# Kernel tuning notes

Hardware: AMD Instinct MI355X
Metric: run time of the kernel (lower is better)

## Reference

```python
import jax, jax.numpy as jnp
import numpy as np

N_STATES = 2048   # number of hidden states
N_OBS = 8192      # emission alphabet size
T = 8192          # sequence length


def setup_inputs() -> dict:
    key = jax.random.key(0)
    k1, k2, k3, k4 = jax.random.split(key, 4)
    Pi_0 = jax.random.uniform(k1, (N_STATES,), jnp.float32)
    Pi_0 = Pi_0 / Pi_0.sum()  # initial distribution
    A = jax.random.uniform(k2, (N_STATES, N_STATES), jnp.float32)
    A = A / A.sum(axis=1, keepdims=True)  # row-stochastic transition matrix
    # emission values scaled so the per-step multiplicative factor has mean ~1,
    # keeping alpha numerically stable over T steps (the raw algorithm never rescales)
    B = jax.random.uniform(k3, (N_STATES, N_OBS), jnp.float32) * 2.0
    se = jax.random.randint(k4, (T,), 0, N_OBS)
    return {"Pi_0": Pi_0, "A": A, "B": B, "se": se}


def reference(Pi_0, A, B, se):
    # HMM forward algorithm:
    #   alpha_0[i] = Pi_0[i] * B[i, se[0]]
    #   alpha_t[i] = (sum_j alpha_{t-1}[j] * A[j, i]) * B[i, se[t]]
    #   return -log(sum_i alpha_T[i])
    Bobs = B[:, se].T            # [T, n_states] emission prob of each observed symbol
    alpha0 = Pi_0 * Bobs[0]      # [n_states]

    def step(alpha, b_t):
        alpha = (alpha @ A) * b_t  # vectorized recurrence: matvec + elementwise
        return alpha, None

    alpha, _ = jax.lax.scan(step, alpha0, Bobs[1:])
    return -jnp.log(jnp.sum(alpha))
```

## Files before the change

### kernel.cpp

```cpp
#include <hip/hip_runtime.h>
#include <math.h>


#define NS    2048
#define NOBS  8192
#define TSEQ  8192
#define NBLK  64
#define NTHR  512
#define OPB   32
#define JPT   128

typedef unsigned long long u64;
typedef unsigned int u32;

#define A_LIST(X) \
  X(0)  X(1)  X(2)  X(3)  X(4)  X(5)  X(6)  X(7)  \
  X(8)  X(9)  X(10) X(11) X(12) X(13) X(14) X(15) \
  X(16) X(17) X(18) X(19) X(20) X(21) X(22) X(23) \
  X(24) X(25) X(26) X(27) X(28) X(29) X(30) X(31)

__global__ void __launch_bounds__(256) init_ws_kernel(u64* aP) {
  const int i = threadIdx.x;
#pragma unroll
  for (int c = 0; c < 16; ++c) {
    __hip_atomic_store(&aP[i * 16 + c], 0ull, __ATOMIC_RELAXED, __HIP_MEMORY_SCOPE_AGENT);
  }
}

__global__ void __launch_bounds__(NTHR, 2) hmm_forward_kernel(
    const float* __restrict__ Pi0,
    const float* __restrict__ A,
    const float* __restrict__ B,
    const int*   __restrict__ se,
    float* __restrict__ out,
    u64*   __restrict__ aP) {
  __shared__ __align__(16) float alpha_sm[NS];
  __shared__ float red[2][NTHR / 64][OPB];

  const int tid    = threadIdx.x;
  const int blk    = blockIdx.x;
  const int w      = tid >> 6;
  const int lane   = tid & 63;
  const int h      = lane >> 5;
  const int o      = lane & 31;
  const int i_mine = blk * OPB + o;
  const int jbase  = (w * 2 + h) * JPT;

#define DECLA(k) float4 Ar##k;
  A_LIST(DECLA)
#define LOADA(k) { const float* ap = A + (size_t)(jbase + 4 * k) * NS + i_mine; \
                   Ar##k.x = ap[0]; Ar##k.y = ap[NS]; Ar##k.z = ap[2 * NS]; Ar##k.w = ap[3 * NS]; }
  A_LIST(LOADA)
#define PIN4(k) asm volatile("" : "+v"(Ar##k.x), "+v"(Ar##k.y), "+v"(Ar##k.z), "+v"(Ar##k.w));
  A_LIST(PIN4)

  {
    const int s0 = se[0];
#pragma unroll
    for (int c = 0; c < 4; ++c) {
      const int i = tid * 4 + c;
      alpha_sm[i] = Pi0[i] * B[(size_t)i * NOBS + s0];
    }
  }
  __syncthreads();

  float bv_next = 0.f;
  if (tid < OPB) bv_next = B[(size_t)i_mine * NOBS + se[1]];
  int sidx_n2 = se[2 < TSEQ ? 2 : TSEQ - 1];

  for (int t = 1; t < TSEQ; ++t) {
    const float bv  = bv_next;
    const int   buf = t & 1;
    if (tid < OPB) bv_next = B[(size_t)i_mine * NOBS + sidx_n2];
    {
      const int tn2 = (t + 2 < TSEQ) ? (t + 2) : (TSEQ - 1);
      sidx_n2 = se[tn2];
    }

    float a0 = 0.f, a1 = 0.f, a2 = 0.f, a3 = 0.f;
#define DOT(k) { const float4 av = *reinterpret_cast<const float4*>(&alpha_sm[jbase + 4 * k]); \
                 a0 = fmaf(Ar##k.x, av.x, a0); a1 = fmaf(Ar##k.y, av.y, a1); \
                 a2 = fmaf(Ar##k.z, av.z, a2); a3 = fmaf(Ar##k.w, av.w, a3); }
    A_LIST(DOT)
    float acc = (a0 + a1) + (a2 + a3);
    acc += __shfl_xor(acc, 32);
    if (lane < 32) red[buf][w][o] = acc;
    __syncthreads();

    if (w == 0) {
      __builtin_amdgcn_s_setprio(1);
      float s = 0.f;
#pragma unroll
      for (int ww = 0; ww < NTHR / 64; ++ww) s += red[buf][ww][o];
      if (lane < 32) {
        const float aval = s * bv;
        const u64 pkt = (u64)__float_as_uint(aval) | ((u64)(u32)t << 32);
        __hip_atomic_store(&aP[(size_t)buf * NS + blk * OPB + o], pkt,
                           __ATOMIC_RELAXED, __HIP_MEMORY_SCOPE_AGENT);
      }
      __builtin_amdgcn_s_setprio(0);
    }

    {
      const u64* src = aP + (size_t)buf * NS + w * 256 + lane * 4;
      u64 q0, q1, q2, q3;
      const u32 tag = (u32)t;
      for (;;) {
        q0 = __hip_atomic_load(&src[0], __ATOMIC_RELAXED, __HIP_MEMORY_SCOPE_AGENT);
        q1 = __hip_atomic_load(&src[1], __ATOMIC_RELAXED, __HIP_MEMORY_SCOPE_AGENT);
        q2 = __hip_atomic_load(&src[2], __ATOMIC_RELAXED, __HIP_MEMORY_SCOPE_AGENT);
        q3 = __hip_atomic_load(&src[3], __ATOMIC_RELAXED, __HIP_MEMORY_SCOPE_AGENT);
        if ((u32)(q0 >> 32) == tag && (u32)(q1 >> 32) == tag &&
            (u32)(q2 >> 32) == tag && (u32)(q3 >> 32) == tag) break;
      }
      float4 v;
      v.x = __uint_as_float((u32)q0);
      v.y = __uint_as_float((u32)q1);
      v.z = __uint_as_float((u32)q2);
      v.w = __uint_as_float((u32)q3);
      *reinterpret_cast<float4*>(&alpha_sm[w * 256 + lane * 4]) = v;
    }
  }

  if (blk == 0) {
    __syncthreads();
    float s = 0.f;
#pragma unroll
    for (int c = 0; c < 4; ++c) s += alpha_sm[4 * tid + c];
#pragma unroll
    for (int off = 32; off > 0; off >>= 1) s += __shfl_xor(s, off);
    if (lane == 0) red[0][w][0] = s;
    __syncthreads();
    if (tid == 0) {
      float S = 0.f;
#pragma unroll
      for (int ww = 0; ww < NTHR / 64; ++ww) S += red[0][ww][0];
      out[0] = -logf(S);
    }
  }
}

extern "C" void kernel_launch(void* const* d_in, const int* in_sizes, int n_in,
                              void* d_out, int out_size, void* d_ws, size_t ws_size,
                              hipStream_t stream) {
  const float* Pi0 = (const float*)d_in[0];
  const float* A   = (const float*)d_in[1];
  const float* B   = (const float*)d_in[2];
  const int*   se  = (const int*)d_in[3];
  float*       out = (float*)d_out;

  u64* aP = (u64*)d_ws;

  init_ws_kernel<<<1, 256, 0, stream>>>(aP);
  hmm_forward_kernel<<<NBLK, NTHR, 0, stream>>>(Pi0, A, B, se, out, aP);
}
```

Measured before the change: 17.42 ms.

## Give each wave four output columns and reduce via wave shuffles

```diff
diff --git a/kernel.cpp b/kernel.cpp
--- a/kernel.cpp
+++ b/kernel.cpp
@@ -7,17 +7,11 @@
 #define TSEQ  8192
 #define NBLK  64
 #define NTHR  512
-#define OPB   32
-#define JPT   128
 
 typedef unsigned long long u64;
 typedef unsigned int u32;
 
-#define A_LIST(X) \
-  X(0)  X(1)  X(2)  X(3)  X(4)  X(5)  X(6)  X(7)  \
-  X(8)  X(9)  X(10) X(11) X(12) X(13) X(14) X(15) \
-  X(16) X(17) X(18) X(19) X(20) X(21) X(22) X(23) \
-  X(24) X(25) X(26) X(27) X(28) X(29) X(30) X(31)
+#define K_LIST(X) X(0) X(1) X(2) X(3) X(4) X(5) X(6) X(7)
 
 __global__ void __launch_bounds__(256) init_ws_kernel(u64* aP) {
   const int i = threadIdx.x;
@@ -34,75 +28,89 @@
     const int*   __restrict__ se,
     float* __restrict__ out,
     u64*   __restrict__ aP) {
-  __shared__ __align__(16) float alpha_sm[NS];
-  __shared__ float red[2][NTHR / 64][OPB];
+  __shared__ __align__(16) float alpha_sm[2][NS];
 
-  const int tid    = threadIdx.x;
-  const int blk    = blockIdx.x;
-  const int w      = tid >> 6;
-  const int lane   = tid & 63;
-  const int h      = lane >> 5;
-  const int o      = lane & 31;
-  const int i_mine = blk * OPB + o;
-  const int jbase  = (w * 2 + h) * JPT;
+  const int tid  = threadIdx.x;
+  const int blk  = blockIdx.x;
+  const int w    = tid >> 6;
+  const int lane = tid & 63;
+  const int gw   = blk * 8 + w;
+  const int c0   = gw * 4;
+  const int jrow = 4 * lane;
 
-#define DECLA(k) float4 Ar##k;
-  A_LIST(DECLA)
-#define LOADA(k) { const float* ap = A + (size_t)(jbase + 4 * k) * NS + i_mine; \
-                   Ar##k.x = ap[0]; Ar##k.y = ap[NS]; Ar##k.z = ap[2 * NS]; Ar##k.w = ap[3 * NS]; }
-  A_LIST(LOADA)
-#define PIN4(k) asm volatile("" : "+v"(Ar##k.x), "+v"(Ar##k.y), "+v"(Ar##k.z), "+v"(Ar##k.w));
-  A_LIST(PIN4)
+#define DECA(k) float4 Ar##k##_0, Ar##k##_1, Ar##k##_2, Ar##k##_3;
+  K_LIST(DECA)
+#define LOADA(k) { const float* ap = A + (size_t)(jrow + 256 * k) * NS + c0; \
+    Ar##k##_0 = *reinterpret_cast<const float4*>(ap); \
+    Ar##k##_1 = *reinterpret_cast<const float4*>(ap + NS); \
+    Ar##k##_2 = *reinterpret_cast<const float4*>(ap + 2 * NS); \
+    Ar##k##_3 = *reinterpret_cast<const float4*>(ap + 3 * NS); }
+  K_LIST(LOADA)
+#define PIN1(f) asm volatile("" : "+v"(f.x), "+v"(f.y), "+v"(f.z), "+v"(f.w));
+#define PINA(k) PIN1(Ar##k##_0) PIN1(Ar##k##_1) PIN1(Ar##k##_2) PIN1(Ar##k##_3)
+  K_LIST(PINA)
 
   {
     const int s0 = se[0];
 #pragma unroll
     for (int c = 0; c < 4; ++c) {
       const int i = tid * 4 + c;
-      alpha_sm[i] = Pi0[i] * B[(size_t)i * NOBS + s0];
+      alpha_sm[0][i] = Pi0[i] * B[(size_t)i * NOBS + s0];
     }
   }
   __syncthreads();
 
   float bv_next = 0.f;
-  if (tid < OPB) bv_next = B[(size_t)i_mine * NOBS + se[1]];
+  if (lane < 4) bv_next = B[(size_t)(c0 + lane) * NOBS + se[1]];
   int sidx_n2 = se[2 < TSEQ ? 2 : TSEQ - 1];
 
   for (int t = 1; t < TSEQ; ++t) {
     const float bv  = bv_next;
     const int   buf = t & 1;
-    if (tid < OPB) bv_next = B[(size_t)i_mine * NOBS + sidx_n2];
+    const float* smb = alpha_sm[buf ^ 1];
+    if (lane < 4) bv_next = B[(size_t)(c0 + lane) * NOBS + sidx_n2];
     {
       const int tn2 = (t + 2 < TSEQ) ? (t + 2) : (TSEQ - 1);
       sidx_n2 = se[tn2];
     }
 
-    float a0 = 0.f, a1 = 0.f, a2 = 0.f, a3 = 0.f;
-#define DOT(k) { const float4 av = *reinterpret_cast<const float4*>(&alpha_sm[jbase + 4 * k]); \
-                 a0 = fmaf(Ar##k.x, av.x, a0); a1 = fmaf(Ar##k.y, av.y, a1); \
-                 a2 = fmaf(Ar##k.z, av.z, a2); a3 = fmaf(Ar##k.w, av.w, a3); }
-    A_LIST(DOT)
-    float acc = (a0 + a1) + (a2 + a3);
-    acc += __shfl_xor(acc, 32);
-    if (lane < 32) red[buf][w][o] = acc;
-    __syncthreads();
+    float4 acc0 = {0.f,0.f,0.f,0.f}, acc1 = {0.f,0.f,0.f,0.f};
+    float4 acc2 = {0.f,0.f,0.f,0.f}, acc3 = {0.f,0.f,0.f,0.f};
+#define DOT(k) { const float4 av = *reinterpret_cast<const float4*>(&smb[jrow + 256 * k]); \
+    acc0.x = fmaf(av.x, Ar##k##_0.x, acc0.x); acc0.y = fmaf(av.x, Ar##k##_0.y, acc0.y); \
+    acc0.z = fmaf(av.x, Ar##k##_0.z, acc0.z); acc0.w = fmaf(av.x, Ar##k##_0.w, acc0.w); \
+    acc1.x = fmaf(av.y, Ar##k##_1.x, acc1.x); acc1.y = fmaf(av.y, Ar##k##_1.y, acc1.y); \
+    acc1.z = fmaf(av.y, Ar##k##_1.z, acc1.z); acc1.w = fmaf(av.y, Ar##k##_1.w, acc1.w); \
+    acc2.x = fmaf(av.z, Ar##k##_2.x, acc2.x); acc2.y = fmaf(av.z, Ar##k##_2.y, acc2.y); \
+    acc2.z = fmaf(av.z, Ar##k##_2.z, acc2.z); acc2.w = fmaf(av.z, Ar##k##_2.w, acc2.w); \
+    acc3.x = fmaf(av.w, Ar##k##_3.x, acc3.x); acc3.y = fmaf(av.w, Ar##k##_3.y, acc3.y); \
+    acc3.z = fmaf(av.w, Ar##k##_3.z, acc3.z); acc3.w = fmaf(av.w, Ar##k##_3.w, acc3.w); }
+    K_LIST(DOT)
+    float4 sv;
+    sv.x = (acc0.x + acc1.x) + (acc2.x + acc3.x);
+    sv.y = (acc0.y + acc1.y) + (acc2.y + acc3.y);
+    sv.z = (acc0.z + acc1.z) + (acc2.z + acc3.z);
+    sv.w = (acc0.w + acc1.w) + (acc2.w + acc3.w);
 
-    if (w == 0) {
-      __builtin_amdgcn_s_setprio(1);
-      float s = 0.f;
 #pragma unroll
-      for (int ww = 0; ww < NTHR / 64; ++ww) s += red[buf][ww][o];
-      if (lane < 32) {
-        const float aval = s * bv;
-        const u64 pkt = (u64)__float_as_uint(aval) | ((u64)(u32)t << 32);
-        __hip_atomic_store(&aP[(size_t)buf * NS + blk * OPB + o], pkt,
-                           __ATOMIC_RELAXED, __HIP_MEMORY_SCOPE_AGENT);
-      }
-      __builtin_amdgcn_s_setprio(0);
+    for (int off = 32; off; off >>= 1) {
+      sv.x += __shfl_xor(sv.x, off);
+      sv.y += __shfl_xor(sv.y, off);
+      sv.z += __shfl_xor(sv.z, off);
+      sv.w += __shfl_xor(sv.w, off);
     }
 
+    u64* base = aP + (size_t)buf * NS;
+    if (lane < 4) {
+      const float vsel = (lane == 0) ? sv.x : (lane == 1) ? sv.y
+                        : (lane == 2) ? sv.z : sv.w;
+      const u64 pkt = (u64)__float_as_uint(vsel * bv) | ((u64)(u32)t << 32);
+      __hip_atomic_store(&base[c0 + lane], pkt, __ATOMIC_RELAXED, __HIP_MEMORY_SCOPE_AGENT);
+    }
+    asm volatile("" ::: "memory");
+
     {
-      const u64* src = aP + (size_t)buf * NS + w * 256 + lane * 4;
+      const u64* src = base + w * 256 + lane * 4;
       u64 q0, q1, q2, q3;
       const u32 tag = (u32)t;
       for (;;) {
@@ -118,23 +126,25 @@
       v.y = __uint_as_float((u32)q1);
       v.z = __uint_as_float((u32)q2);
       v.w = __uint_as_float((u32)q3);
-      *reinterpret_cast<float4*>(&alpha_sm[w * 256 + lane * 4]) = v;
+      *reinterpret_cast<float4*>(&alpha_sm[buf][w * 256 + lane * 4]) = v;
     }
+    __syncthreads();
   }
 
   if (blk == 0) {
-    __syncthreads();
+    const float* smf = alpha_sm[(TSEQ - 1) & 1];
     float s = 0.f;
 #pragma unroll
-    for (int c = 0; c < 4; ++c) s += alpha_sm[4 * tid + c];
+    for (int c = 0; c < 4; ++c) s += smf[tid * 4 + c];
 #pragma unroll
-    for (int off = 32; off > 0; off >>= 1) s += __shfl_xor(s, off);
-    if (lane == 0) red[0][w][0] = s;
+    for (int off = 32; off; off >>= 1) s += __shfl_xor(s, off);
+    __syncthreads();
+    if (lane == 0) alpha_sm[0][w] = s;
     __syncthreads();
     if (tid == 0) {
       float S = 0.f;
 #pragma unroll
-      for (int ww = 0; ww < NTHR / 64; ++ww) S += red[0][ww][0];
+      for (int ww = 0; ww < 8; ++ww) S += alpha_sm[0][ww];
       out[0] = -logf(S);
     }
   }
```

Result: slower. 32.68 ms (+87.6%).
